# Optimization experiments

Measured on AMD Instinct MI355X. Metric: run time of the kernel, lower is better.

Reference implementation:

```python
import jax, jax.numpy as jnp
import numpy as np


def conv1x1(x, W, b):
    # 1x1 Conv2d == per-pixel linear over channels. x: [B,C,H,W], W: [O,C], b: [O]
    return jnp.einsum('oc,bchw->bohw', W, x) + b[None, :, None, None]


def setup_inputs() -> dict:
    key = jax.random.key(0)
    ks = jax.random.split(key, 18)
    B, C, Hd, H, W = 16, 64, 64, 32, 32
    s = 0.05
    f = jax.random.normal
    return {
        'h': f(ks[0], (B, C, H, W), jnp.float32),
        'm': f(ks[1], (B, C, H, W), jnp.float32),
        'Wq': f(ks[2], (Hd, C), jnp.float32) * s,
        'bq': f(ks[3], (Hd,), jnp.float32) * s,
        'Wk': f(ks[4], (Hd, C), jnp.float32) * s,
        'bk': f(ks[5], (Hd,), jnp.float32) * s,
        'Wk2': f(ks[6], (Hd, C), jnp.float32) * s,
        'bk2': f(ks[7], (Hd,), jnp.float32) * s,
        'Wv': f(ks[8], (C, C), jnp.float32) * s,
        'bv': f(ks[9], (C,), jnp.float32) * s,
        'Wv2': f(ks[10], (C, C), jnp.float32) * s,
        'bv2': f(ks[11], (C,), jnp.float32) * s,
        'Wz': f(ks[12], (2 * C, 2 * C), jnp.float32) * s,
        'bz': f(ks[13], (2 * C,), jnp.float32) * s,
        'Wm': f(ks[14], (3 * C, 3 * C), jnp.float32) * s,
        'bm': f(ks[15], (3 * C,), jnp.float32) * s,
    }


def reference(h, m, Wq, bq, Wk, bk, Wk2, bk2, Wv, bv, Wv2, bv2, Wz, bz, Wm, bm):
    B, C, H, W = h.shape
    Hd = Wq.shape[0]
    N = H * W
    # Shared query from h
    Q_h = conv1x1(h, Wq, bq).reshape(B, Hd, N).transpose(0, 2, 1)  # [B,N,Hd]
    # Self-attention branch over h
    K_h = conv1x1(h, Wk, bk).reshape(B, Hd, N)                     # [B,Hd,N]
    A_h = jax.nn.softmax(jnp.einsum('bnd,bdm->bnm', Q_h, K_h), axis=-1)  # [B,N,N]
    V_h = conv1x1(h, Wv, bv).reshape(B, C, N)                      # [B,C,N]
    Z_h = jnp.einsum('bnm,bcm->bcn', A_h, V_h).reshape(B, C, H, W)
    # Cross-attention branch over memory m (same query Q_h)
    K_m = conv1x1(m, Wk2, bk2).reshape(B, Hd, N)
    A_m = jax.nn.softmax(jnp.einsum('bnd,bdm->bnm', Q_h, K_m), axis=-1)
    V_m = conv1x1(m, Wv2, bv2).reshape(B, C, N)
    Z_m = jnp.einsum('bnm,bcm->bcn', A_m, V_m).reshape(B, C, H, W)
    # Fuse and gated memory update
    Z = conv1x1(jnp.concatenate([Z_h, Z_m], axis=1), Wz, bz)       # [B,2C,H,W]
    combined = conv1x1(jnp.concatenate([Z, h], axis=1), Wm, bm)    # [B,3C,H,W]
    mo, mg, mi = combined[:, :C], combined[:, C:2 * C], combined[:, 2 * C:]
    mi = jax.nn.sigmoid(mi)
    new_m = (1 - mi) * m + mi * jnp.tanh(mg)
    new_h = jax.nn.sigmoid(mo) * new_m
    return (new_h, new_m)
```

## Files before the change

### kernel.cpp

```cpp
#include <hip/hip_runtime.h>

typedef unsigned short u16;
typedef unsigned int u32;
typedef __attribute__((ext_vector_type(8))) short bf16x8;
typedef __attribute__((ext_vector_type(4))) short bf16x4;
typedef __attribute__((ext_vector_type(4))) float f32x4;

#define MFMA(a, b, c) __builtin_amdgcn_mfma_f32_16x16x32_bf16((a), (b), (c), 0, 0, 0)
#define MFMA16(a, b, c) __builtin_amdgcn_mfma_f32_16x16x16bf16_1k((a), (b), (c), 0, 0, 0)

static __device__ __forceinline__ u16 f2bf(float x) {
  u32 u = __float_as_uint(x);
  u += 0x7FFFu + ((u >> 16) & 1u);
  return (u16)(u >> 16);
}
static __device__ __forceinline__ u32 packbf_t(float hi, float lo) {
  return __builtin_amdgcn_perm(__float_as_uint(hi), __float_as_uint(lo), 0x07060302u);
}
static __device__ __forceinline__ u32 packbf(float lo, float hi) {
  return (u32)f2bf(lo) | ((u32)f2bf(hi) << 16);
}

__global__ __launch_bounds__(256) void proj_kernel(
    const float* __restrict__ h, const float* __restrict__ m_,
    const float* __restrict__ bq, const float* __restrict__ bk,
    const float* __restrict__ bk2, const float* __restrict__ bv,
    const float* __restrict__ bv2,
    const float* __restrict__ Wq, const float* __restrict__ Wk,
    const float* __restrict__ Wk2, const float* __restrict__ Wv,
    const float* __restrict__ Wv2,
    const float* __restrict__ Wz, const float* __restrict__ Wm,
    const float* __restrict__ bm,
    u16* __restrict__ Qb, u16* __restrict__ Khb, u16* __restrict__ Kmb,
    u16* __restrict__ Vhb, u16* __restrict__ Vmb, u16* __restrict__ hbuf,
    u16* __restrict__ Wzb, u16* __restrict__ Wmb, float* __restrict__ bmp)
{
  const int tid = threadIdx.x;
  const int b = blockIdx.y, n0 = blockIdx.x * 64, z = blockIdx.z;

  {
    const int gid = (blockIdx.z * 256 + blockIdx.y * 16 + blockIdx.x) * 256 + tid;
    if (gid < 16384) {
      Wzb[gid] = f2bf(Wz[gid]);
    } else if (gid < 53248) {
      const int e = gid - 16384;
      const int p = e / 192, k = e % 192;
      const int hb2 = p / 96, r1 = p % 96, ctl = r1 / 48, r2 = r1 % 48;
      const int g = r2 >> 4, mm = r2 & 15;
      const int o = g * 64 + (hb2 * 2 + ctl) * 16 + mm;
      Wmb[p * 192 + k] = f2bf(Wm[o * 192 + k]);
    } else if (gid < 53440) {
      const int p = gid - 53248;
      const int hb2 = p / 96, r1 = p % 96, ctl = r1 / 48, r2 = r1 % 48;
      const int g = r2 >> 4, mm = r2 & 15;
      const int o = g * 64 + (hb2 * 2 + ctl) * 16 + mm;
      bmp[p] = bm[o];
    }
  }

  __shared__ __align__(16) u16 xt[64][72];
  const float* __restrict__ X = (z >= 3) ? m_ : h;

  {
    const int px = tid & 63, c0 = (tid >> 6) * 16;
#pragma unroll
    for (int i = 0; i < 8; ++i) {
      const int c = c0 + 2 * i;
      const float f0 = X[(b * 64 + c) * 1024 + n0 + px];
      const float f1 = X[(b * 64 + c + 1) * 1024 + n0 + px];
      *(u32*)&xt[px][c] = packbf(f0, f1);
    }
  }
  __syncthreads();

  const int lane = tid & 63, w = tid >> 6;
  const int mm = lane & 15, q = lane >> 4;

  const bf16x8 xa0 = *(const bf16x8*)&xt[w * 16 + mm][q * 8];
  const bf16x8 xa1 = *(const bf16x8*)&xt[w * 16 + mm][32 + q * 8];

  auto ldw8 = [&](const float* Wf, int row, int col0) {
    const float4 a = *(const float4*)(Wf + row * 64 + col0);
    const float4 bb = *(const float4*)(Wf + row * 64 + col0 + 4);
    union { u32 u[4]; bf16x8 v; } r;
    r.u[0] = packbf(a.x, a.y);
    r.u[1] = packbf(a.z, a.w);
    r.u[2] = packbf(bb.x, bb.y);
    r.u[3] = packbf(bb.z, bb.w);
    return r.v;
  };

  auto qk_store = [&](u16* dst, const float* Wf, const float* bias) {
#pragma unroll
    for (int ot = 0; ot < 4; ++ot) {
      const bf16x8 wb0 = ldw8(Wf, ot * 16 + mm, q * 8);
      const bf16x8 wb1 = ldw8(Wf, ot * 16 + mm, 32 + q * 8);
      const float4 b4 = *(const float4*)(bias + ot * 16 + q * 4);
      f32x4 d = {b4.x, b4.y, b4.z, b4.w};
      d = MFMA(wb0, xa0, d);
      d = MFMA(wb1, xa1, d);
      uint2 val;
      val.x = packbf(d[0], d[1]);
      val.y = packbf(d[2], d[3]);
      *(uint2*)(dst + (b * 1024 + n0 + w * 16 + mm) * 64 + ot * 16 + q * 4) = val;
    }
  };
  auto v_store = [&](u16* dst, const float* Wf, const float* bias) {
#pragma unroll
    for (int ot = 0; ot < 4; ++ot) {
      const bf16x8 wb0 = ldw8(Wf, ot * 16 + mm, q * 8);
      const bf16x8 wb1 = ldw8(Wf, ot * 16 + mm, 32 + q * 8);
      const float bb = bias[ot * 16 + mm];
      f32x4 d = {bb, bb, bb, bb};
      d = MFMA(xa0, wb0, d);
      d = MFMA(xa1, wb1, d);
      uint2 val;
      val.x = packbf(d[0], d[1]);
      val.y = packbf(d[2], d[3]);
      *(uint2*)(dst + b * 65536 + blockIdx.x * 4096 + (ot * 16 + mm) * 64 +
                w * 16 + q * 4) = val;
    }
  };

  if (z == 0) {
    qk_store(Qb, Wq, bq);
    const int px = tid >> 2, sg = tid & 3;
    u32* dst = (u32*)(hbuf + (b * 1024 + n0 + px) * 64 + sg * 16);
    const u16* srcr = &xt[px][sg * 16];
#pragma unroll
    for (int j = 0; j < 8; ++j) dst[j] = *(const u32*)(srcr + 2 * j);
  } else if (z == 1) {
    qk_store(Khb, Wk, bk);
  } else if (z == 2) {
    v_store(Vhb, Wv, bv);
  } else if (z == 3) {
    qk_store(Kmb, Wk2, bk2);
  } else {
    v_store(Vmb, Wv2, bv2);
  }
}

__global__ __launch_bounds__(256) void attn_kernel(
    const u16* __restrict__ Qb, const u16* __restrict__ Khb,
    const u16* __restrict__ Kmb, const u16* __restrict__ Vhb,
    const u16* __restrict__ Vmb, u16* __restrict__ Ztb)
{
  const int id = blockIdx.x;
  const int b = id & 15;
  const int br = (id >> 4) & 1;
  const int qh = id >> 5;
  const u16* __restrict__ K = (br ? Kmb : Khb) + b * 65536;
  const u16* __restrict__ V = (br ? Vmb : Vhb) + b * 65536;

  __shared__ __align__(16) u16 pool[18432];
  __shared__ float rsw[4][64];
  u16* const Kl = pool;
  u16* const Vl = pool + 9216;

  const int tid = threadIdx.x, w = tid >> 6, lane = tid & 63;
  const int mm = lane & 15, q = lane >> 4;
  const int q0 = qh * 64;

  bf16x8 qb0[4], qb1[4];
#pragma unroll
  for (int qt = 0; qt < 4; ++qt) {
    const u16* Qp = Qb + (b * 1024 + q0 + qt * 16 + mm) * 64;
    qb0[qt] = *(const bf16x8*)(Qp + q * 8);
    qb1[qt] = *(const bf16x8*)(Qp + 32 + q * 8);
  }

  f32x4 z[4][4];
#pragma unroll
  for (int qt = 0; qt < 4; ++qt)
#pragma unroll
    for (int ct = 0; ct < 4; ++ct) z[qt][ct] = (f32x4){0.f, 0.f, 0.f, 0.f};
  float rp[4] = {0.f, 0.f, 0.f, 0.f};

  const int so0 = (tid >> 3) * 72 + (tid & 7) * 8;
  const int so1 = so0 + 32 * 72;

  uint4 ka0, ka1, va0, va1;
  uint4 kb0, kb1, vb0, vb1;
  auto ld = [&](int kc, uint4& r0, uint4& r1, uint4& s0, uint4& s1) {
    const u16* Ks = K + kc * 4096;
    const u16* Vs = V + kc * 4096;
    r0 = *(const uint4*)(Ks + tid * 8);
    r1 = *(const uint4*)(Ks + tid * 8 + 2048);
    s0 = *(const uint4*)(Vs + tid * 8);
    s1 = *(const uint4*)(Vs + tid * 8 + 2048);
  };
  auto st = [&](int buf, const uint4& r0, const uint4& r1, const uint4& s0,
                const uint4& s1) {
    u16* Kd = Kl + buf * 4608;
    u16* Vd = Vl + buf * 4608;
    *(uint4*)(Kd + so0) = r0;
    *(uint4*)(Kd + so1) = r1;
    *(uint4*)(Vd + so0) = s0;
    *(uint4*)(Vd + so1) = s1;
  };

  auto compute = [&](int cur) {
    const u16* Kc = Kl + cur * 4608;
    const u16* Vc = Vl + cur * 4608;
    const bf16x8 kf0 = *(const bf16x8*)(Kc + (w * 16 + mm) * 72 + q * 8);
    const bf16x8 kf1 = *(const bf16x8*)(Kc + (w * 16 + mm) * 72 + 32 + q * 8);
    bf16x4 vf[4];
#pragma unroll
    for (int ct = 0; ct < 4; ++ct)
      vf[ct] = *(const bf16x4*)(Vc + (ct * 16 + mm) * 72 + w * 16 + q * 4);

#pragma unroll
    for (int qt = 0; qt < 4; ++qt) {
      f32x4 s = {0.f, 0.f, 0.f, 0.f};
      s = MFMA(kf0, qb0[qt], s);
      s = MFMA(kf1, qb1[qt], s);
      const float e0 = __expf(s[0]), e1 = __expf(s[1]);
      const float e2 = __expf(s[2]), e3 = __expf(s[3]);
      rp[qt] += (e0 + e1) + (e2 + e3);
      union { u32 u[2]; bf16x4 v; } pb;
      pb.u[0] = packbf_t(e1, e0);
      pb.u[1] = packbf_t(e3, e2);
#pragma unroll
      for (int ct = 0; ct < 4; ++ct) z[qt][ct] = MFMA16(vf[ct], pb.v, z[qt][ct]);
    }
  };

  ld(0, ka0, ka1, va0, va1);
  st(0, ka0, ka1, va0, va1);
  ld(1, ka0, ka1, va0, va1);
  __syncthreads();

#pragma unroll 1
  for (int kc = 0; kc < 16; kc += 2) {
    if (kc + 2 < 16) ld(kc + 2, kb0, kb1, vb0, vb1);
    compute(0);
    st(1, ka0, ka1, va0, va1);
    __syncthreads();
    if (kc + 3 < 16) ld(kc + 3, ka0, ka1, va0, va1);
    compute(1);
    if (kc + 2 < 16) st(0, kb0, kb1, vb0, vb1);
    __syncthreads();
  }

  u16* const zcb = pool;
#pragma unroll
  for (int qt = 0; qt < 4; ++qt) {
    float v = rp[qt];
    v += __shfl_xor(v, 16);
    v += __shfl_xor(v, 32);
    if (q == 0) rsw[w][qt * 16 + mm] = v;
#pragma unroll
    for (int ct = 0; ct < 4; ++ct) {
      uint2 val;
      val.x = packbf_t(z[qt][ct][1], z[qt][ct][0]);
      val.y = packbf_t(z[qt][ct][3], z[qt][ct][2]);
      *(uint2*)(zcb + w * 4352 + (qt * 16 + mm) * 68 + ct * 16 + q * 4) = val;
    }
  }
  __syncthreads();

  const int c2 = tid & 31, qr = tid >> 5;
#pragma unroll
  for (int i = 0; i < 8; ++i) {
    const int query = qr + i * 8;
    const float rt = rsw[0][query] + rsw[1][query] + rsw[2][query] + rsw[3][query];
    const float rinv = __builtin_amdgcn_rcpf(rt);
    float vlo = 0.f, vhi = 0.f;
#pragma unroll
    for (int ww = 0; ww < 4; ++ww) {
      const u32 u = *(const u32*)(zcb + ww * 4352 + query * 68 + c2 * 2);
      vlo += __uint_as_float(u << 16);
      vhi += __uint_as_float(u & 0xffff0000u);
    }
    vlo *= rinv;
    vhi *= rinv;
    *(u32*)(Ztb + (b * 1024 + q0 + query) * 128 + br * 64 + c2 * 2) = packbf_t(vhi, vlo);
  }
}

__global__ __launch_bounds__(256) void tail_kernel(
    const u16* __restrict__ Ztb, const u16* __restrict__ hbuf,
    const float* __restrict__ m_, const u16* __restrict__ Wzb,
    const float* __restrict__ bz, const u16* __restrict__ Wmb,
    const float* __restrict__ bmp, float* __restrict__ out)
{
  const int b = blockIdx.y, n0 = blockIdx.x * 16;
  __shared__ __align__(16) u16 zp[16][136];
  const int tid = threadIdx.x, lane = tid & 63, wv = tid >> 6;
  const int mm = lane & 15, q = lane >> 4;

  {
    bf16x8 za[4];
#pragma unroll
    for (int ks = 0; ks < 4; ++ks)
      za[ks] = *(const bf16x8*)(Ztb + (b * 1024 + n0 + mm) * 128 + ks * 32 + q * 8);
#pragma unroll
    for (int ot = 0; ot < 2; ++ot) {
      const int o0 = wv * 32 + ot * 16;
      const float4 b4 = *(const float4*)(bz + o0 + q * 4);
      f32x4 d = {b4.x, b4.y, b4.z, b4.w};
#pragma unroll
      for (int ks = 0; ks < 4; ++ks) {
        const bf16x8 wb = *(const bf16x8*)(Wzb + (o0 + mm) * 128 + ks * 32 + q * 8);
        d = MFMA(wb, za[ks], d);
      }
      uint2 val;
      val.x = packbf(d[0], d[1]);
      val.y = packbf(d[2], d[3]);
      *(uint2*)&zp[mm][o0 + q * 4] = val;
    }
  }
  __syncthreads();

  {
    bf16x8 fa[6];
#pragma unroll
    for (int ks = 0; ks < 4; ++ks)
      fa[ks] = *(const bf16x8*)&zp[mm][ks * 32 + q * 8];
    {
      const u16* hp = hbuf + (b * 1024 + n0 + mm) * 64;
      fa[4] = *(const bf16x8*)(hp + q * 8);
      fa[5] = *(const bf16x8*)(hp + 32 + q * 8);
    }
    f32x4 dd[3];
#pragma unroll
    for (int j = 0; j < 3; ++j) {
      const int p = wv * 48 + j * 16 + mm;
      const float bb = bmp[p];
      f32x4 d = {bb, bb, bb, bb};
#pragma unroll
      for (int ks = 0; ks < 6; ++ks) {
        const bf16x8 wb = *(const bf16x8*)(Wmb + p * 192 + ks * 32 + q * 8);
        d = MFMA(fa[ks], wb, d);
      }
      dd[j] = d;
    }
    const int c = wv * 16 + mm;
    const int px = n0 + q * 4;
    const float4 mold = *(const float4*)(m_ + (b * 64 + c) * 1024 + px);
    float4 nh, nm;
#pragma unroll
    for (int r = 0; r < 4; ++r) {
      const float xo = dd[0][r];
      const float xg = dd[1][r];
      const float xi = dd[2][r];
      const float si = __builtin_amdgcn_rcpf(1.f + __expf(-xi));
      const float th = 1.f - 2.f * __builtin_amdgcn_rcpf(__expf(2.f * xg) + 1.f);
      const float so = __builtin_amdgcn_rcpf(1.f + __expf(-xo));
      const float mo = ((const float*)&mold)[r];
      const float nmv = (1.f - si) * mo + si * th;
      ((float*)&nm)[r] = nmv;
      ((float*)&nh)[r] = so * nmv;
    }
    *(float4*)(out + (b * 64 + c) * 1024 + px) = nh;
    *(float4*)(out + 1048576 + (b * 64 + c) * 1024 + px) = nm;
  }
}

extern "C" void kernel_launch(void* const* d_in, const int* in_sizes, int n_in,
                              void* d_out, int out_size, void* d_ws, size_t ws_size,
                              hipStream_t stream) {
  const float* h   = (const float*)d_in[0];
  const float* m   = (const float*)d_in[1];
  const float* Wq  = (const float*)d_in[2];
  const float* bq  = (const float*)d_in[3];
  const float* Wk  = (const float*)d_in[4];
  const float* bk  = (const float*)d_in[5];
  const float* Wk2 = (const float*)d_in[6];
  const float* bk2 = (const float*)d_in[7];
  const float* Wv  = (const float*)d_in[8];
  const float* bv  = (const float*)d_in[9];
  const float* Wv2 = (const float*)d_in[10];
  const float* bv2 = (const float*)d_in[11];
  const float* Wz  = (const float*)d_in[12];
  const float* bz  = (const float*)d_in[13];
  const float* Wm  = (const float*)d_in[14];
  const float* bm  = (const float*)d_in[15];
  float* out = (float*)d_out;

  char* ws = (char*)d_ws;
  const size_t MB = 1024 * 1024;
  u16* Qb   = (u16*)(ws + 0 * MB);
  u16* Khb  = (u16*)(ws + 2 * MB);
  u16* Kmb  = (u16*)(ws + 4 * MB);
  u16* Vhb  = (u16*)(ws + 6 * MB);
  u16* Vmb  = (u16*)(ws + 8 * MB);
  u16* hbuf = (u16*)(ws + 10 * MB);
  u16* Ztb  = (u16*)(ws + 12 * MB);
  u16* Wzb  = (u16*)(ws + 16 * MB + 40960);
  u16* Wmb  = (u16*)(ws + 16 * MB + 73728);
  float* bmp = (float*)(ws + 16 * MB + 147456);

  proj_kernel<<<dim3(16, 16, 5), 256, 0, stream>>>(
      h, m, bq, bk, bk2, bv, bv2, Wq, Wk, Wk2, Wv, Wv2, Wz, Wm, bm,
      Qb, Khb, Kmb, Vhb, Vmb, hbuf, Wzb, Wmb, bmp);
  attn_kernel<<<512, 256, 0, stream>>>(Qb, Khb, Kmb, Vhb, Vmb, Ztb);
  tail_kernel<<<dim3(64, 16), 256, 0, stream>>>(Ztb, hbuf, m, Wzb, bz, Wmb, bmp, out);
}
```

Baseline: 140.4 us.

## Give each warp a private K/V LDS arena to drop block-wide barriers in attention

The V projection now writes its output in a per-warp tiled layout (16-key slices contiguous), so each warp in the attention kernel can load only its own 16 keys of K and V into a private double-buffered LDS region. This removes the two __syncthreads per chunk pair in the key loop, since warps no longer share staged tiles. The cost is a larger LDS footprint (21504 vs 18432 u16), which may lower occupancy. Correctness depends on wavefront-local LDS ordering without explicit barriers and on producer and consumer agreeing on the new V layout.

```diff
diff --git a/kernel.cpp b/kernel.cpp
--- a/kernel.cpp
+++ b/kernel.cpp
@@ -117,8 +117,8 @@
       uint2 val;
       val.x = packbf(d[0], d[1]);
       val.y = packbf(d[2], d[3]);
-      *(uint2*)(dst + b * 65536 + blockIdx.x * 4096 + (ot * 16 + mm) * 64 +
-                w * 16 + q * 4) = val;
+      *(uint2*)(dst + b * 65536 + blockIdx.x * 4096 + w * 1024 +
+                (ot * 16 + mm) * 16 + q * 4) = val;
     }
   };
 
@@ -152,14 +152,14 @@
   const u16* __restrict__ K = (br ? Kmb : Khb) + b * 65536;
   const u16* __restrict__ V = (br ? Vmb : Vhb) + b * 65536;
 
-  __shared__ __align__(16) u16 pool[18432];
+  __shared__ __align__(16) u16 pool[21504];
   __shared__ float rsw[4][64];
-  u16* const Kl = pool;
-  u16* const Vl = pool + 9216;
 
   const int tid = threadIdx.x, w = tid >> 6, lane = tid & 63;
   const int mm = lane & 15, q = lane >> 4;
   const int q0 = qh * 64;
+
+  u16* const warena = pool + w * 5376;
 
   bf16x8 qb0[4], qb1[4];
 #pragma unroll
@@ -176,38 +176,33 @@
     for (int ct = 0; ct < 4; ++ct) z[qt][ct] = (f32x4){0.f, 0.f, 0.f, 0.f};
   float rp[4] = {0.f, 0.f, 0.f, 0.f};
 
-  const int so0 = (tid >> 3) * 72 + (tid & 7) * 8;
-  const int so1 = so0 + 32 * 72;
-
-  uint4 ka0, ka1, va0, va1;
-  uint4 kb0, kb1, vb0, vb1;
-  auto ld = [&](int kc, uint4& r0, uint4& r1, uint4& s0, uint4& s1) {
-    const u16* Ks = K + kc * 4096;
-    const u16* Vs = V + kc * 4096;
-    r0 = *(const uint4*)(Ks + tid * 8);
-    r1 = *(const uint4*)(Ks + tid * 8 + 2048);
-    s0 = *(const uint4*)(Vs + tid * 8);
-    s1 = *(const uint4*)(Vs + tid * 8 + 2048);
-  };
-  auto st = [&](int buf, const uint4& r0, const uint4& r1, const uint4& s0,
-                const uint4& s1) {
-    u16* Kd = Kl + buf * 4608;
-    u16* Vd = Vl + buf * 4608;
-    *(uint4*)(Kd + so0) = r0;
-    *(uint4*)(Kd + so1) = r1;
-    *(uint4*)(Vd + so0) = s0;
-    *(uint4*)(Vd + so1) = s1;
-  };
-
-  auto compute = [&](int cur) {
-    const u16* Kc = Kl + cur * 4608;
-    const u16* Vc = Vl + cur * 4608;
-    const bf16x8 kf0 = *(const bf16x8*)(Kc + (w * 16 + mm) * 72 + q * 8);
-    const bf16x8 kf1 = *(const bf16x8*)(Kc + (w * 16 + mm) * 72 + 32 + q * 8);
+  uint4 k0, k1, v0, v1;
+  auto ldg = [&](int kc) {
+    const u16* Ks = K + kc * 4096 + w * 1024 + lane * 16;
+    const u16* Vs = V + kc * 4096 + w * 1024 + lane * 16;
+    k0 = *(const uint4*)Ks;
+    k1 = *(const uint4*)(Ks + 8);
+    v0 = *(const uint4*)Vs;
+    v1 = *(const uint4*)(Vs + 8);
+  };
+  auto stl = [&](int buf) {
+    u16* Kd = warena + buf * 2688 + (lane >> 2) * 72 + (lane & 3) * 16;
+    u16* Vd = warena + buf * 2688 + 1152 + lane * 24;
+    *(uint4*)Kd = k0;
+    *(uint4*)(Kd + 8) = k1;
+    *(uint4*)Vd = v0;
+    *(uint4*)(Vd + 8) = v1;
+  };
+
+  auto compute = [&](int buf) {
+    const u16* Kt = warena + buf * 2688;
+    const u16* Vt = warena + buf * 2688 + 1152;
+    const bf16x8 kf0 = *(const bf16x8*)(Kt + mm * 72 + q * 8);
+    const bf16x8 kf1 = *(const bf16x8*)(Kt + mm * 72 + 32 + q * 8);
     bf16x4 vf[4];
 #pragma unroll
     for (int ct = 0; ct < 4; ++ct)
-      vf[ct] = *(const bf16x4*)(Vc + (ct * 16 + mm) * 72 + w * 16 + q * 4);
+      vf[ct] = *(const bf16x4*)(Vt + (ct * 16 + mm) * 24 + q * 4);
 
 #pragma unroll
     for (int qt = 0; qt < 4; ++qt) {
@@ -225,22 +220,22 @@
     }
   };
 
-  ld(0, ka0, ka1, va0, va1);
-  st(0, ka0, ka1, va0, va1);
-  ld(1, ka0, ka1, va0, va1);
+  ldg(0);
+  stl(0);
+  ldg(1);
+
+  int cur = 0;
+#pragma unroll 1
+  for (int kc = 0; kc < 16; ++kc) {
+    compute(cur);
+    if (kc < 15) {
+      stl(cur ^ 1);
+      if (kc < 14) ldg(kc + 2);
+      cur ^= 1;
+    }
+  }
+
   __syncthreads();
-
-#pragma unroll 1
-  for (int kc = 0; kc < 16; kc += 2) {
-    if (kc + 2 < 16) ld(kc + 2, kb0, kb1, vb0, vb1);
-    compute(0);
-    st(1, ka0, ka1, va0, va1);
-    __syncthreads();
-    if (kc + 3 < 16) ld(kc + 3, ka0, ka1, va0, va1);
-    compute(1);
-    if (kc + 2 < 16) st(0, kb0, kb1, vb0, vb1);
-    __syncthreads();
-  }
 
   u16* const zcb = pool;
 #pragma unroll
```

Measured after the change: 138.7 us. About the same (-1.2%).
